# Kernel tuning notes

Hardware: AMD Instinct MI355X
Metric: run time of the kernel (lower is better)

Reference implementation:

```python
import jax, jax.numpy as jnp
import numpy as np

N_NODES = 50000
N_EDGES = 800000
VOCAB = 4096
EMB = 128
HID = 128


def glorot(key, shape):
    limit = float(np.sqrt(6.0 / (shape[0] + shape[1])))
    return jax.random.uniform(key, shape, jnp.float32, -limit, limit)


def setup_inputs() -> dict:
    key = jax.random.key(0)
    k = jax.random.split(key, 6)
    x = jax.random.randint(k[0], (N_NODES, 1), 0, VOCAB, dtype=jnp.int64)
    edge_index = jax.random.randint(k[1], (2, N_EDGES), 0, N_NODES, dtype=jnp.int64)
    # Embedding init: normal(0, dim^-0.5)
    emb = jax.random.normal(k[2], (VOCAB, EMB), jnp.float32) * (EMB ** -0.5)
    W1 = glorot(k[3], (EMB, 2 * HID))
    b1 = jnp.zeros((2 * HID,), jnp.float32)
    W2 = glorot(k[4], (2 * HID, HID))
    b2 = jnp.zeros((HID,), jnp.float32)
    return {"x": x, "edge_index": edge_index, "emb": emb,
            "W1": W1, "b1": b1, "W2": W2, "b2": b2}


def _gcn_conv(h, src, dst, norm, W, b):
    # PyG GCNConv: transform then degree-normalized aggregate over A + I.
    h = h @ W                                   # [N, F_out]
    msg = norm[:, None] * h[src]                # [(E+N), F_out] gather
    out = jax.ops.segment_sum(msg, dst, num_segments=N_NODES)  # scatter-add
    return out + b


def _edges_with_self_loops_and_norm(edge_index):
    loop = jnp.arange(N_NODES, dtype=edge_index.dtype)
    src = jnp.concatenate([edge_index[0], loop])
    dst = jnp.concatenate([edge_index[1], loop])
    deg = jax.ops.segment_sum(jnp.ones_like(dst, jnp.float32), dst,
                              num_segments=N_NODES)
    inv_sqrt = jnp.where(deg > 0, deg ** -0.5, 0.0)
    norm = inv_sqrt[src] * inv_sqrt[dst]        # [(E+N)]
    return src, dst, norm


def reference(x, edge_index, emb, W1, b1, W2, b2):
    src, dst, norm = _edges_with_self_loops_and_norm(edge_index)
    h = emb[x[:, 0]]                            # embedding lookup + squeeze(1)
    h = jax.nn.relu(_gcn_conv(h, src, dst, norm, W1, b1))
    h = _gcn_conv(h, src, dst, norm, W2, b2)
    return h
```

## Files before the change

### kernel.cpp

```cpp
#include <hip/hip_runtime.h>


constexpr int FEAT = 128;
constexpr int HID2 = 256;
constexpr int CAP  = 64;

typedef __attribute__((ext_vector_type(8))) __bf16 bf16x8;
typedef __attribute__((ext_vector_type(4))) float f32x4;
union FragU { uint4 u; bf16x8 b; };

__device__ inline void split_bf16_rne(float v, unsigned short& h, unsigned short& l) {
  unsigned u = __float_as_uint(v);
  unsigned short hh = (unsigned short)((u + 0x7FFFu + ((u >> 16) & 1u)) >> 16);
  float r = v - __uint_as_float(((unsigned)hh) << 16);
  unsigned u2 = __float_as_uint(r);
  unsigned short ll = (unsigned short)((u2 + 0x7FFFu + ((u2 >> 16) & 1u)) >> 16);
  h = hh; l = ll;
}

__device__ inline void split_trunc1(float v, unsigned short& h, unsigned short& l) {
  unsigned u = __float_as_uint(v);
  h = (unsigned short)(u >> 16);
  float r = v - __uint_as_float(u & 0xFFFF0000u);
  l = (unsigned short)(__float_as_uint(r) >> 16);
}


__global__ __launch_bounds__(256) void k_init_prep(int* cnt, int N, int nblkN,
    const float* __restrict__ W1, const float* __restrict__ W2,
    unsigned short* __restrict__ w1s_hi, unsigned short* __restrict__ w1s_lo,
    unsigned short* __restrict__ w2s_hi, unsigned short* __restrict__ w2s_lo) {
  int b = blockIdx.x;
  if (b < nblkN) {
    int i = b * 256 + threadIdx.x;
    if (i < N) cnt[i] = 0;
    return;
  }
  int idx = (b - nblkN) * 256 + threadIdx.x;
  unsigned short h, l;
  if (idx < FEAT * HID2) {
    int k = idx >> 8, n = idx & 255;
    split_bf16_rne(W1[idx], h, l);
    int t = n >> 4, lr = n & 15, kc = k >> 5, quad = (k >> 3) & 3, j = k & 7;
    int us = (((t * 4 + kc) * 64 + quad * 16 + lr) << 3) + j;
    w1s_hi[us] = h;
    w1s_lo[us] = l;
  } else {
    int jj = idx - FEAT * HID2;
    int k = jj >> 7, n = jj & 127;
    split_bf16_rne(W2[jj], h, l);
    int t = n >> 4, lr = n & 15, kc = k >> 5, quad = (k >> 3) & 3, j = k & 7;
    int us = (((t * 8 + kc) * 64 + quad * 16 + lr) << 3) + j;
    w2s_hi[us] = h;
    w2s_lo[us] = l;
  }
}


__global__ __launch_bounds__(256) void k_bucket(const int* __restrict__ src,
    const int* __restrict__ dst, int* cnt, unsigned short* csr, int E, int chunkN) {
  int g = blockIdx.x & 7;
  int e = (blockIdx.x >> 3) * 256 + threadIdx.x;
  if (e >= E) return;
  int d = dst[e];
  int lo = g * chunkN;
  if (d >= lo && d < lo + chunkN) {
    int pos = atomicAdd(&cnt[d], 1);
    if (pos < CAP) csr[d * CAP + pos] = (unsigned short)src[e];
  }
}


__global__ __launch_bounds__(256) void k_gather_l1(const int* __restrict__ x,
    const float* __restrict__ emb, const int* __restrict__ cnt,
    const unsigned short* __restrict__ csr,
    unsigned short* __restrict__ aggf_hi, unsigned short* __restrict__ aggf_lo,
    int N) {
  int half  = blockIdx.x & 1;
  int chunk = blockIdx.x >> 1;
  int node  = chunk * 16 + (threadIdx.x >> 4);
  if (node >= N) return;
  int c4 = half * 64 + (threadIdx.x & 15) * 4;
  int degN = cnt[node];
  float wd = rsqrtf((float)(degN + 1));
  int deg = degN > CAP ? CAP : degN;

  float4 acc = *reinterpret_cast<const float4*>(&emb[(long long)x[node] * FEAT + c4]);
  acc.x *= wd; acc.y *= wd; acc.z *= wd; acc.w *= wd;

  const unsigned short* row = csr + node * CAP;
  int j = 0;
  for (; j + 7 < deg; j += 8) {
    uint4 c8 = *reinterpret_cast<const uint4*>(row + j);
    int s[8] = {(int)(c8.x & 0xFFFF), (int)(c8.x >> 16),
                (int)(c8.y & 0xFFFF), (int)(c8.y >> 16),
                (int)(c8.z & 0xFFFF), (int)(c8.z >> 16),
                (int)(c8.w & 0xFFFF), (int)(c8.w >> 16)};
    int xs[8];
    float ws[8];
    #pragma unroll
    for (int q = 0; q < 8; ++q) xs[q] = x[s[q]];
    #pragma unroll
    for (int q = 0; q < 8; ++q) ws[q] = rsqrtf((float)(cnt[s[q]] + 1));
    float4 r[8];
    #pragma unroll
    for (int q = 0; q < 8; ++q)
      r[q] = *reinterpret_cast<const float4*>(&emb[(long long)xs[q] * FEAT + c4]);
    #pragma unroll
    for (int q = 0; q < 8; ++q) {
      acc.x += ws[q] * r[q].x; acc.y += ws[q] * r[q].y;
      acc.z += ws[q] * r[q].z; acc.w += ws[q] * r[q].w;
    }
  }
  if (j + 3 < deg) {
    uint2 c4e = *reinterpret_cast<const uint2*>(row + j);
    int s[4] = {(int)(c4e.x & 0xFFFF), (int)(c4e.x >> 16),
                (int)(c4e.y & 0xFFFF), (int)(c4e.y >> 16)};
    int xs[4];
    float ws[4];
    #pragma unroll
    for (int q = 0; q < 4; ++q) xs[q] = x[s[q]];
    #pragma unroll
    for (int q = 0; q < 4; ++q) ws[q] = rsqrtf((float)(cnt[s[q]] + 1));
    float4 r[4];
    #pragma unroll
    for (int q = 0; q < 4; ++q)
      r[q] = *reinterpret_cast<const float4*>(&emb[(long long)xs[q] * FEAT + c4]);
    #pragma unroll
    for (int q = 0; q < 4; ++q) {
      acc.x += ws[q] * r[q].x; acc.y += ws[q] * r[q].y;
      acc.z += ws[q] * r[q].z; acc.w += ws[q] * r[q].w;
    }
    j += 4;
  }
  for (; j < deg; ++j) {
    int s = row[j];
    float w = rsqrtf((float)(cnt[s] + 1));
    float4 a = *reinterpret_cast<const float4*>(&emb[(long long)x[s] * FEAT + c4]);
    acc.x += w * a.x; acc.y += w * a.y; acc.z += w * a.z; acc.w += w * a.w;
  }

  acc.x *= wd; acc.y *= wd; acc.z *= wd; acc.w *= wd;
  ushort4 h4, l4;
  split_bf16_rne(acc.x, h4.x, l4.x);
  split_bf16_rne(acc.y, h4.y, l4.y);
  split_bf16_rne(acc.z, h4.z, l4.z);
  split_bf16_rne(acc.w, h4.w, l4.w);

  int T = node >> 4, lr = node & 15;
  int kc = c4 >> 5, quad = (c4 >> 3) & 3, sub = c4 & 7;
  long long us = (((long long)(T * 4 + kc) * 64 + quad * 16 + lr) << 3) + sub;
  *reinterpret_cast<ushort4*>(aggf_hi + us) = h4;
  *reinterpret_cast<ushort4*>(aggf_lo + us) = l4;
}


__global__ __launch_bounds__(256) void k_gather_l2(const float* __restrict__ hs2s,
    const int* __restrict__ cnt, const unsigned short* __restrict__ csr,
    const float* __restrict__ bias, float* __restrict__ out, int N, int Np) {
  int slice = blockIdx.x & 7;
  int chunk = blockIdx.x >> 3;
  int node  = chunk * 64 + (threadIdx.x >> 2);
  if (node >= N) return;
  int sc4 = (threadIdx.x & 3) * 4;
  const float* sl = hs2s + (long long)slice * Np * 16;

  float4 acc = *reinterpret_cast<const float4*>(&sl[node * 16 + sc4]);
  const unsigned short* row = csr + node * CAP;
  int degN = cnt[node];
  int deg = degN > CAP ? CAP : degN;
  int j = 0;
  for (; j + 15 < deg; j += 16) {
    uint4 c0 = *reinterpret_cast<const uint4*>(row + j);
    uint4 c1 = *reinterpret_cast<const uint4*>(row + j + 8);
    int s[16] = {(int)(c0.x & 0xFFFF), (int)(c0.x >> 16),
                 (int)(c0.y & 0xFFFF), (int)(c0.y >> 16),
                 (int)(c0.z & 0xFFFF), (int)(c0.z >> 16),
                 (int)(c0.w & 0xFFFF), (int)(c0.w >> 16),
                 (int)(c1.x & 0xFFFF), (int)(c1.x >> 16),
                 (int)(c1.y & 0xFFFF), (int)(c1.y >> 16),
                 (int)(c1.z & 0xFFFF), (int)(c1.z >> 16),
                 (int)(c1.w & 0xFFFF), (int)(c1.w >> 16)};
    float4 r[16];
    #pragma unroll
    for (int q = 0; q < 16; ++q)
      r[q] = *reinterpret_cast<const float4*>(&sl[s[q] * 16 + sc4]);
    #pragma unroll
    for (int q = 0; q < 16; ++q) {
      acc.x += r[q].x; acc.y += r[q].y; acc.z += r[q].z; acc.w += r[q].w;
    }
  }
  if (j + 7 < deg) {
    uint4 c8 = *reinterpret_cast<const uint4*>(row + j);
    int s[8] = {(int)(c8.x & 0xFFFF), (int)(c8.x >> 16),
                (int)(c8.y & 0xFFFF), (int)(c8.y >> 16),
                (int)(c8.z & 0xFFFF), (int)(c8.z >> 16),
                (int)(c8.w & 0xFFFF), (int)(c8.w >> 16)};
    float4 r[8];
    #pragma unroll
    for (int q = 0; q < 8; ++q)
      r[q] = *reinterpret_cast<const float4*>(&sl[s[q] * 16 + sc4]);
    #pragma unroll
    for (int q = 0; q < 8; ++q) {
      acc.x += r[q].x; acc.y += r[q].y; acc.z += r[q].z; acc.w += r[q].w;
    }
    j += 8;
  }
  if (j + 3 < deg) {
    uint2 c4e = *reinterpret_cast<const uint2*>(row + j);
    int s[4] = {(int)(c4e.x & 0xFFFF), (int)(c4e.x >> 16),
                (int)(c4e.y & 0xFFFF), (int)(c4e.y >> 16)};
    float4 r[4];
    #pragma unroll
    for (int q = 0; q < 4; ++q)
      r[q] = *reinterpret_cast<const float4*>(&sl[s[q] * 16 + sc4]);
    #pragma unroll
    for (int q = 0; q < 4; ++q) {
      acc.x += r[q].x; acc.y += r[q].y; acc.z += r[q].z; acc.w += r[q].w;
    }
    j += 4;
  }
  for (; j < deg; ++j) {
    float4 a = *reinterpret_cast<const float4*>(&sl[row[j] * 16 + sc4]);
    acc.x += a.x; acc.y += a.y; acc.z += a.z; acc.w += a.w;
  }

  float w = rsqrtf((float)(degN + 1));
  int col = slice * 16 + sc4;
  float4 b = *reinterpret_cast<const float4*>(&bias[col]);
  acc.x = acc.x * w + b.x; acc.y = acc.y * w + b.y;
  acc.z = acc.z * w + b.z; acc.w = acc.w * w + b.w;
  *reinterpret_cast<float4*>(&out[(long long)node * FEAT + col]) = acc;
}


__global__ __launch_bounds__(256, 2) void k_mlp(
    const uint4* __restrict__ aggf_hi, const uint4* __restrict__ aggf_lo,
    const uint4* __restrict__ w1s_hi, const uint4* __restrict__ w1s_lo,
    const uint4* __restrict__ w2s_hi, const uint4* __restrict__ w2s_lo,
    const float* __restrict__ b1, const int* __restrict__ cnt,
    float* __restrict__ hs2s, int N, int Np) {
  __shared__ __align__(16) unsigned short h1h[32 * 256];
  __shared__ __align__(16) unsigned short h1l[32 * 256];

  int tid  = threadIdx.x;
  int wave = tid >> 6, lane = tid & 63, quad = lane >> 4, lr = lane & 15;
  int m0 = blockIdx.x * 32;
  int Tb = blockIdx.x * 2;

  FragU a1h[2][4], a1l[2][4];
  #pragma unroll
  for (int rt = 0; rt < 2; ++rt)
    #pragma unroll
    for (int kc = 0; kc < 4; ++kc) {
      a1h[rt][kc].u = aggf_hi[(long long)((Tb + rt) * 4 + kc) * 64 + lane];
      a1l[rt][kc].u = aggf_lo[(long long)((Tb + rt) * 4 + kc) * 64 + lane];
    }

  FragU bh[2][4], bl[2][4];
  auto loadB1 = [&](int t, int buf) {
    #pragma unroll
    for (int kc = 0; kc < 4; ++kc) {
      bh[buf][kc].u = w1s_hi[(t * 4 + kc) * 64 + lane];
      bl[buf][kc].u = w1s_lo[(t * 4 + kc) * 64 + lane];
    }
  };
  auto comp1 = [&](int t, int buf) {
    f32x4 hh[2], hl[2], lh[2];
    #pragma unroll
    for (int rt = 0; rt < 2; ++rt) {
      hh[rt] = f32x4{0.f, 0.f, 0.f, 0.f};
      hl[rt] = f32x4{0.f, 0.f, 0.f, 0.f};
      lh[rt] = f32x4{0.f, 0.f, 0.f, 0.f};
    }
    #pragma unroll
    for (int kc = 0; kc < 4; ++kc)
      #pragma unroll
      for (int rt = 0; rt < 2; ++rt) {
        hh[rt] = __builtin_amdgcn_mfma_f32_16x16x32_bf16(a1h[rt][kc].b, bh[buf][kc].b, hh[rt], 0, 0, 0);
        hl[rt] = __builtin_amdgcn_mfma_f32_16x16x32_bf16(a1h[rt][kc].b, bl[buf][kc].b, hl[rt], 0, 0, 0);
        lh[rt] = __builtin_amdgcn_mfma_f32_16x16x32_bf16(a1l[rt][kc].b, bh[buf][kc].b, lh[rt], 0, 0, 0);
      }
    float bias = b1[t * 16 + lr];
    int c = t * 2 + (lr >> 3), jj = lr & 7;
    #pragma unroll
    for (int rt = 0; rt < 2; ++rt)
      #pragma unroll
      for (int r = 0; r < 4; ++r) {
        float v = hh[rt][r] + hl[rt][r] + lh[rt][r] + bias;
        v = v > 0.f ? v : 0.f;
        int row = rt * 16 + quad * 4 + r;
        int us = ((row * 32 + (c ^ (row & 7))) << 3) + jj;
        unsigned short sh, sl;
        split_trunc1(v, sh, sl);
        h1h[us] = sh;
        h1l[us] = sl;
      }
  };

  int t0 = wave * 4;
  loadB1(t0, 0);
  #pragma unroll
  for (int i = 0; i < 4; ++i) {
    if (i < 3) loadB1(t0 + i + 1, (i + 1) & 1);
    comp1(t0 + i, i & 1);
  }

  __syncthreads();

  float inv_r[2][4];
  #pragma unroll
  for (int rt = 0; rt < 2; ++rt)
    #pragma unroll
    for (int r = 0; r < 4; ++r) {
      int g = m0 + rt * 16 + quad * 4 + r;
      inv_r[rt][r] = rsqrtf((float)(cnt[g < N ? g : N - 1] + 1));
    }

  #pragma unroll
  for (int ti = 0; ti < 2; ++ti) {
    int t2 = wave * 2 + ti;
    f32x4 hh[2], hl[2], lh[2];
    #pragma unroll
    for (int rt = 0; rt < 2; ++rt) {
      hh[rt] = f32x4{0.f, 0.f, 0.f, 0.f};
      hl[rt] = f32x4{0.f, 0.f, 0.f, 0.f};
      lh[rt] = f32x4{0.f, 0.f, 0.f, 0.f};
    }
    #pragma unroll
    for (int kh = 0; kh < 2; ++kh) {
      FragU b2h[4], b2l[4];
      #pragma unroll
      for (int kc = 0; kc < 4; ++kc) {
        b2h[kc].u = w2s_hi[(t2 * 8 + kh * 4 + kc) * 64 + lane];
        b2l[kc].u = w2s_lo[(t2 * 8 + kh * 4 + kc) * 64 + lane];
      }
      FragU a2h[2][4], a2l[2][4];
      #pragma unroll
      for (int rt = 0; rt < 2; ++rt) {
        int row = rt * 16 + lr;
        #pragma unroll
        for (int kc = 0; kc < 4; ++kc) {
          int pc = (kh * 16 + kc * 4 + quad) ^ (row & 7);
          a2h[rt][kc].u = *reinterpret_cast<const uint4*>(&h1h[(row * 32 + pc) << 3]);
          a2l[rt][kc].u = *reinterpret_cast<const uint4*>(&h1l[(row * 32 + pc) << 3]);
        }
      }
      #pragma unroll
      for (int kc = 0; kc < 4; ++kc)
        #pragma unroll
        for (int rt = 0; rt < 2; ++rt) {
          hh[rt] = __builtin_amdgcn_mfma_f32_16x16x32_bf16(a2h[rt][kc].b, b2h[kc].b, hh[rt], 0, 0, 0);
          hl[rt] = __builtin_amdgcn_mfma_f32_16x16x32_bf16(a2h[rt][kc].b, b2l[kc].b, hl[rt], 0, 0, 0);
          lh[rt] = __builtin_amdgcn_mfma_f32_16x16x32_bf16(a2l[rt][kc].b, b2h[kc].b, lh[rt], 0, 0, 0);
        }
    }
    float* sl = hs2s + (long long)t2 * Np * 16;
    #pragma unroll
    for (int rt = 0; rt < 2; ++rt)
      #pragma unroll
      for (int r = 0; r < 4; ++r) {
        int g = m0 + rt * 16 + quad * 4 + r;
        if (g < N)
          sl[g * 16 + lr] = (hh[rt][r] + hl[rt][r] + lh[rt][r]) * inv_r[rt][r];
      }
  }
}


extern "C" void kernel_launch(void* const* d_in, const int* in_sizes, int n_in,
                              void* d_out, int out_size, void* d_ws, size_t ws_size,
                              hipStream_t stream) {
  const int*   x   = (const int*)d_in[0];
  const int*   ei  = (const int*)d_in[1];
  const float* emb = (const float*)d_in[2];
  const float* W1  = (const float*)d_in[3];
  const float* b1  = (const float*)d_in[4];
  const float* W2  = (const float*)d_in[5];
  const float* b2  = (const float*)d_in[6];
  float* out = (float*)d_out;

  const int N  = in_sizes[0];
  const int E  = in_sizes[1] / 2;
  const int nblk_mlp = (N + 31) / 32;
  const int Np = nblk_mlp * 32;
  const int chunkN = (N + 7) / 8;
  const int* src = ei;
  const int* dst = ei + E;

  int* cnt = (int*)d_ws;
  unsigned short* csr = (unsigned short*)(cnt + N);
  unsigned short* aggf_hi = csr + (long long)N * CAP;
  unsigned short* aggf_lo = aggf_hi + (long long)Np * FEAT;
  float* hs2s   = (float*)(aggf_lo + (long long)Np * FEAT);
  unsigned short* w1s_hi = (unsigned short*)(hs2s + (long long)Np * FEAT);
  unsigned short* w1s_lo = w1s_hi + FEAT * HID2;
  unsigned short* w2s_hi = w1s_lo + FEAT * HID2;
  unsigned short* w2s_lo = w2s_hi + FEAT * HID2;

  const int nblk_N  = (N + 255) / 256;
  const int nblk_E8 = ((E + 255) / 256) * 8;
  const int nblk_g1 = ((N + 15) / 16) * 2;
  const int nblk_g2 = ((N + 63) / 64) * 8;

  k_init_prep<<<nblk_N + 256, 256, 0, stream>>>(cnt, N, nblk_N, W1, W2,
                                                w1s_hi, w1s_lo, w2s_hi, w2s_lo);
  k_bucket<<<nblk_E8, 256, 0, stream>>>(src, dst, cnt, csr, E, chunkN);

  k_gather_l1<<<nblk_g1, 256, 0, stream>>>(x, emb, cnt, csr,
                                           aggf_hi, aggf_lo, N);
  k_mlp<<<nblk_mlp, 256, 0, stream>>>((const uint4*)aggf_hi, (const uint4*)aggf_lo,
                                      (const uint4*)w1s_hi, (const uint4*)w1s_lo,
                                      (const uint4*)w2s_hi, (const uint4*)w2s_lo,
                                      b1, cnt, hs2s, N, Np);
  k_gather_l2<<<nblk_g2, 256, 0, stream>>>(hs2s, cnt, csr, b2, out, N, Np);
}
```

Baseline: 237.6 us.

## Store layer-2 transformed features in fp16 with two 64-wide slices

The MLP kernel now writes the pre-aggregation layer-2 features as fp16 instead of fp32, laid out as two 64-column halves rather than eight 16-column slices. The layer-2 gather reads 16-byte fp16 vectors (8 features per thread, 8 threads per node) and accumulates in fp32, and block-to-node mapping is remapped into quarters. This halves the gather's random-access bytes and the intermediate's footprint, so it fits better in cache. The cost is lost precision in the intermediate, which could affect accuracy tolerance.

```diff
diff --git a/kernel.cpp b/kernel.cpp
--- a/kernel.cpp
+++ b/kernel.cpp
@@ -7,7 +7,10 @@
 
 typedef __attribute__((ext_vector_type(8))) __bf16 bf16x8;
 typedef __attribute__((ext_vector_type(4))) float f32x4;
+typedef __attribute__((ext_vector_type(8))) _Float16 f16x8;
+typedef __attribute__((ext_vector_type(4))) _Float16 f16x4;
 union FragU { uint4 u; bf16x8 b; };
+union H16 { _Float16 f; unsigned short u; };
 
 __device__ inline void split_bf16_rne(float v, unsigned short& h, unsigned short& l) {
   unsigned u = __float_as_uint(v);
@@ -155,17 +158,27 @@
 }
 
 
-__global__ __launch_bounds__(256) void k_gather_l2(const float* __restrict__ hs2s,
+__global__ __launch_bounds__(256) void k_gather_l2(
+    const unsigned short* __restrict__ hs2h,
     const int* __restrict__ cnt, const unsigned short* __restrict__ csr,
     const float* __restrict__ bias, float* __restrict__ out, int N, int Np) {
-  int slice = blockIdx.x & 7;
-  int chunk = blockIdx.x >> 3;
-  int node  = chunk * 64 + (threadIdx.x >> 2);
+  int g    = blockIdx.x & 7;
+  int half = g >> 2, qtr = g & 3;
+  int Nq   = (N + 3) >> 2;
+  int local = (blockIdx.x >> 3) * 32 + (threadIdx.x >> 3);
+  if (local >= Nq) return;
+  int node = qtr * Nq + local;
   if (node >= N) return;
-  int sc4 = (threadIdx.x & 3) * 4;
-  const float* sl = hs2s + (long long)slice * Np * 16;
-
-  float4 acc = *reinterpret_cast<const float4*>(&sl[node * 16 + sc4]);
+  int f8 = (threadIdx.x & 7) * 8;
+  const unsigned short* sl = hs2h + (long long)half * Np * 64;
+
+  f32x4 a0, a1;
+  {
+    f16x8 v = *reinterpret_cast<const f16x8*>(sl + (long long)node * 64 + f8);
+    a0 = __builtin_convertvector(__builtin_shufflevector(v, v, 0, 1, 2, 3), f32x4);
+    a1 = __builtin_convertvector(__builtin_shufflevector(v, v, 4, 5, 6, 7), f32x4);
+  }
+
   const unsigned short* row = csr + node * CAP;
   int degN = cnt[node];
   int deg = degN > CAP ? CAP : degN;
@@ -181,13 +194,14 @@
                  (int)(c1.y & 0xFFFF), (int)(c1.y >> 16),
                  (int)(c1.z & 0xFFFF), (int)(c1.z >> 16),
                  (int)(c1.w & 0xFFFF), (int)(c1.w >> 16)};
-    float4 r[16];
+    f16x8 r[16];
     #pragma unroll
     for (int q = 0; q < 16; ++q)
-      r[q] = *reinterpret_cast<const float4*>(&sl[s[q] * 16 + sc4]);
+      r[q] = *reinterpret_cast<const f16x8*>(sl + (long long)s[q] * 64 + f8);
     #pragma unroll
     for (int q = 0; q < 16; ++q) {
-      acc.x += r[q].x; acc.y += r[q].y; acc.z += r[q].z; acc.w += r[q].w;
+      a0 += __builtin_convertvector(__builtin_shufflevector(r[q], r[q], 0, 1, 2, 3), f32x4);
+      a1 += __builtin_convertvector(__builtin_shufflevector(r[q], r[q], 4, 5, 6, 7), f32x4);
     }
   }
   if (j + 7 < deg) {
@@ -196,13 +210,14 @@
                 (int)(c8.y & 0xFFFF), (int)(c8.y >> 16),
                 (int)(c8.z & 0xFFFF), (int)(c8.z >> 16),
                 (int)(c8.w & 0xFFFF), (int)(c8.w >> 16)};
-    float4 r[8];
+    f16x8 r[8];
     #pragma unroll
     for (int q = 0; q < 8; ++q)
-      r[q] = *reinterpret_cast<const float4*>(&sl[s[q] * 16 + sc4]);
+      r[q] = *reinterpret_cast<const f16x8*>(sl + (long long)s[q] * 64 + f8);
     #pragma unroll
     for (int q = 0; q < 8; ++q) {
-      acc.x += r[q].x; acc.y += r[q].y; acc.z += r[q].z; acc.w += r[q].w;
+      a0 += __builtin_convertvector(__builtin_shufflevector(r[q], r[q], 0, 1, 2, 3), f32x4);
+      a1 += __builtin_convertvector(__builtin_shufflevector(r[q], r[q], 4, 5, 6, 7), f32x4);
     }
     j += 8;
   }
@@ -210,27 +225,31 @@
     uint2 c4e = *reinterpret_cast<const uint2*>(row + j);
     int s[4] = {(int)(c4e.x & 0xFFFF), (int)(c4e.x >> 16),
                 (int)(c4e.y & 0xFFFF), (int)(c4e.y >> 16)};
-    float4 r[4];
+    f16x8 r[4];
     #pragma unroll
     for (int q = 0; q < 4; ++q)
-      r[q] = *reinterpret_cast<const float4*>(&sl[s[q] * 16 + sc4]);
+      r[q] = *reinterpret_cast<const f16x8*>(sl + (long long)s[q] * 64 + f8);
     #pragma unroll
     for (int q = 0; q < 4; ++q) {
-      acc.x += r[q].x; acc.y += r[q].y; acc.z += r[q].z; acc.w += r[q].w;
+      a0 += __builtin_convertvector(__builtin_shufflevector(r[q], r[q], 0, 1, 2, 3), f32x4);
+      a1 += __builtin_convertvector(__builtin_shufflevector(r[q], r[q], 4, 5, 6, 7), f32x4);
     }
     j += 4;
   }
   for (; j < deg; ++j) {
-    float4 a = *reinterpret_cast<const float4*>(&sl[row[j] * 16 + sc4]);
-    acc.x += a.x; acc.y += a.y; acc.z += a.z; acc.w += a.w;
+    f16x8 v = *reinterpret_cast<const f16x8*>(sl + (long long)row[j] * 64 + f8);
+    a0 += __builtin_convertvector(__builtin_shufflevector(v, v, 0, 1, 2, 3), f32x4);
+    a1 += __builtin_convertvector(__builtin_shufflevector(v, v, 4, 5, 6, 7), f32x4);
   }
 
   float w = rsqrtf((float)(degN + 1));
-  int col = slice * 16 + sc4;
-  float4 b = *reinterpret_cast<const float4*>(&bias[col]);
-  acc.x = acc.x * w + b.x; acc.y = acc.y * w + b.y;
-  acc.z = acc.z * w + b.z; acc.w = acc.w * w + b.w;
-  *reinterpret_cast<float4*>(&out[(long long)node * FEAT + col]) = acc;
+  int col = half * 64 + f8;
+  f32x4 b0 = *reinterpret_cast<const f32x4*>(&bias[col]);
+  f32x4 b1v = *reinterpret_cast<const f32x4*>(&bias[col + 4]);
+  a0 = a0 * w + b0;
+  a1 = a1 * w + b1v;
+  *reinterpret_cast<f32x4*>(&out[(long long)node * FEAT + col]) = a0;
+  *reinterpret_cast<f32x4*>(&out[(long long)node * FEAT + col + 4]) = a1;
 }
 
 
@@ -239,7 +258,7 @@
     const uint4* __restrict__ w1s_hi, const uint4* __restrict__ w1s_lo,
     const uint4* __restrict__ w2s_hi, const uint4* __restrict__ w2s_lo,
     const float* __restrict__ b1, const int* __restrict__ cnt,
-    float* __restrict__ hs2s, int N, int Np) {
+    unsigned short* __restrict__ hs2h, int N, int Np) {
   __shared__ __align__(16) unsigned short h1h[32 * 256];
   __shared__ __align__(16) unsigned short h1l[32 * 256];
 
@@ -355,14 +374,18 @@
           lh[rt] = __builtin_amdgcn_mfma_f32_16x16x32_bf16(a2l[rt][kc].b, b2h[kc].b, lh[rt], 0, 0, 0);
         }
     }
-    float* sl = hs2s + (long long)t2 * Np * 16;
+    unsigned short* sl2 = hs2h + (long long)(t2 >> 2) * Np * 64 + (t2 & 3) * 16;
     #pragma unroll
     for (int rt = 0; rt < 2; ++rt)
       #pragma unroll
       for (int r = 0; r < 4; ++r) {
         int g = m0 + rt * 16 + quad * 4 + r;
-        if (g < N)
-          sl[g * 16 + lr] = (hh[rt][r] + hl[rt][r] + lh[rt][r]) * inv_r[rt][r];
+        if (g < N) {
+          float v = (hh[rt][r] + hl[rt][r] + lh[rt][r]) * inv_r[rt][r];
+          H16 cv;
+          cv.f = (_Float16)v;
+          sl2[(long long)g * 64 + lr] = cv.u;
+        }
       }
   }
 }
@@ -392,16 +415,17 @@
   unsigned short* csr = (unsigned short*)(cnt + N);
   unsigned short* aggf_hi = csr + (long long)N * CAP;
   unsigned short* aggf_lo = aggf_hi + (long long)Np * FEAT;
-  float* hs2s   = (float*)(aggf_lo + (long long)Np * FEAT);
-  unsigned short* w1s_hi = (unsigned short*)(hs2s + (long long)Np * FEAT);
+  unsigned short* hs2h = aggf_lo + (long long)Np * FEAT;
+  unsigned short* w1s_hi = hs2h + (long long)Np * FEAT;
   unsigned short* w1s_lo = w1s_hi + FEAT * HID2;
   unsigned short* w2s_hi = w1s_lo + FEAT * HID2;
   unsigned short* w2s_lo = w2s_hi + FEAT * HID2;
 
+  const int Nq = (N + 3) / 4;
   const int nblk_N  = (N + 255) / 256;
   const int nblk_E8 = ((E + 255) / 256) * 8;
   const int nblk_g1 = ((N + 15) / 16) * 2;
-  const int nblk_g2 = ((N + 63) / 64) * 8;
+  const int nblk_g2 = ((Nq + 31) / 32) * 8;
 
   k_init_prep<<<nblk_N + 256, 256, 0, stream>>>(cnt, N, nblk_N, W1, W2,
                                                 w1s_hi, w1s_lo, w2s_hi, w2s_lo);
@@ -412,6 +436,6 @@
   k_mlp<<<nblk_mlp, 256, 0, stream>>>((const uint4*)aggf_hi, (const uint4*)aggf_lo,
                                       (const uint4*)w1s_hi, (const uint4*)w1s_lo,
                                       (const uint4*)w2s_hi, (const uint4*)w2s_lo,
-                                      b1, cnt, hs2s, N, Np);
-  k_gather_l2<<<nblk_g2, 256, 0, stream>>>(hs2s, cnt, csr, b2, out, N, Np);
-}
+                                      b1, cnt, hs2h, N, Np);
+  k_gather_l2<<<nblk_g2, 256, 0, stream>>>(hs2h, cnt, csr, b2, out, N, Np);
+}
```

Result: faster. 232.7 us (-2.1%).
